# Performance work log

Hardware: AMD Instinct MI355X
Metric: run time of the kernel (lower is better)

Reference implementation:

```python
import jax, jax.numpy as jnp
import numpy as np

N_FEAT = 128
N_HID = 32
N_HEAD = 4
N_CLASS = 40
HIDDEN = N_HID * N_HEAD  # 128
N_NODES = 50000
N_EDGES = 800000


def _gat_layer(x, src, dst, W, a_s, a_d, b, heads, out_ch, concat):
    # PyG GATConv (eval mode, self-loops already appended to src/dst).
    N = x.shape[0]
    h = (x @ W).reshape(N, heads, out_ch)                      # [N,H,C]
    es = jnp.einsum('nhc,hc->nh', h, a_s)                      # alpha_src per node
    ed = jnp.einsum('nhc,hc->nh', h, a_d)                      # alpha_dst per node
    e = jax.nn.leaky_relu(es[src] + ed[dst], 0.2)              # [E,H]
    m = jax.ops.segment_max(e, dst, num_segments=N)            # segment softmax over dst
    p = jnp.exp(e - m[dst])
    s = jax.ops.segment_sum(p, dst, num_segments=N)
    alpha = p / s[dst]                                         # [E,H]
    out = jax.ops.segment_sum(h[src] * alpha[:, :, None], dst, num_segments=N)  # [N,H,C]
    out = out.reshape(N, heads * out_ch) if concat else out.mean(axis=1)
    return out + b


def setup_inputs() -> dict:
    key = jax.random.key(0)
    ks = jax.random.split(key, 16)
    sc = 0.1
    inp = {
        'x': jax.random.normal(ks[0], (N_NODES, N_FEAT), jnp.float32),
        'edge_index': jax.random.randint(ks[1], (2, N_EDGES), 0, N_NODES, jnp.int32),
        'W0': jax.random.normal(ks[2], (N_FEAT, HIDDEN), jnp.float32) * sc,
        'as0': jax.random.normal(ks[3], (N_HEAD, N_HID), jnp.float32) * sc,
        'ad0': jax.random.normal(ks[4], (N_HEAD, N_HID), jnp.float32) * sc,
        'b0': jnp.zeros((HIDDEN,), jnp.float32),
        'W1': jax.random.normal(ks[5], (HIDDEN, HIDDEN), jnp.float32) * sc,
        'as1': jax.random.normal(ks[6], (N_HEAD, N_HID), jnp.float32) * sc,
        'ad1': jax.random.normal(ks[7], (N_HEAD, N_HID), jnp.float32) * sc,
        'b1': jnp.zeros((HIDDEN,), jnp.float32),
        'W2': jax.random.normal(ks[8], (HIDDEN, HIDDEN), jnp.float32) * sc,
        'as2': jax.random.normal(ks[9], (N_HEAD, N_HID), jnp.float32) * sc,
        'ad2': jax.random.normal(ks[10], (N_HEAD, N_HID), jnp.float32) * sc,
        'b2': jnp.zeros((HIDDEN,), jnp.float32),
        'Wo': jax.random.normal(ks[11], (HIDDEN, N_CLASS), jnp.float32) * sc,
        'aso': jax.random.normal(ks[12], (1, N_CLASS), jnp.float32) * sc,
        'ado': jax.random.normal(ks[13], (1, N_CLASS), jnp.float32) * sc,
        'bo': jnp.zeros((N_CLASS,), jnp.float32),
    }
    return inp


def reference(x, edge_index, W0, as0, ad0, b0, W1, as1, ad1, b1, W2, as2, ad2, b2, Wo, aso, ado, bo):
    N = x.shape[0]
    loops = jnp.arange(N, dtype=edge_index.dtype)              # add_self_loops=True
    src = jnp.concatenate([edge_index[0], loops])
    dst = jnp.concatenate([edge_index[1], loops])
    # dropout is a no-op in eval mode
    x = jax.nn.elu(_gat_layer(x, src, dst, W0, as0, ad0, b0, N_HEAD, N_HID, True))
    for (W, a1, a2, b) in ((W1, as1, ad1, b1), (W2, as2, ad2, b2)):
        h = _gat_layer(x, src, dst, W, a1, a2, b, N_HEAD, N_HID, True)
        x = jax.nn.elu(h + x)                                  # 'res' skip connection
    out = _gat_layer(x, src, dst, Wo, aso, ado, bo, 1, N_CLASS, False)
    return out
```

## Files before the change

kernel.cpp:

```cpp
#include <hip/hip_runtime.h>
#include <hip/hip_bf16.h>

#define N_FEAT 128
#define HIDDEN 128
#define NHEAD  4
#define NHID   32
#define NCLASS 40


__global__ __launch_bounds__(256) void k_zero(int* __restrict__ p, int n) {
  int i = blockIdx.x * 256 + threadIdx.x;
  if (i < n) p[i] = 0;
}

__global__ __launch_bounds__(256) void k_hist(const int* __restrict__ dst, int* __restrict__ counts, int E) {
  int e = blockIdx.x * 256 + threadIdx.x;
  if (e < E) atomicAdd(&counts[dst[e]], 1);
}

__device__ __forceinline__ int block_incl_scan_256(int v, int* sm) {
  int t = threadIdx.x;
  sm[t] = v;
  __syncthreads();
  #pragma unroll
  for (int d = 1; d < 256; d <<= 1) {
    int u = (t >= d) ? sm[t - d] : 0;
    __syncthreads();
    sm[t] += u;
    __syncthreads();
  }
  return sm[t];
}

__global__ __launch_bounds__(256) void k_bsum(const int* __restrict__ counts, int* __restrict__ bsum, int N) {
  __shared__ int sm[256];
  int i = blockIdx.x * 256 + threadIdx.x;
  int v = (i < N) ? counts[i] : 0;
  int incl = block_incl_scan_256(v, sm);
  if (threadIdx.x == 255) bsum[blockIdx.x] = incl;
}

__global__ __launch_bounds__(256) void k_scanb(const int* __restrict__ bsum, int* __restrict__ boff,
                                               int* __restrict__ offs, int nblk, int N) {
  __shared__ int sm[256];
  int t = threadIdx.x;
  int v = (t < nblk) ? bsum[t] : 0;
  int incl = block_incl_scan_256(v, sm);
  if (t < nblk) boff[t] = incl - v;
  if (t == 255) offs[N] = incl;
}

__global__ __launch_bounds__(256) void k_scanfin(const int* __restrict__ counts, const int* __restrict__ boff,
                                                 int* __restrict__ offs, int* __restrict__ cursor, int N) {
  __shared__ int sm[256];
  int b = blockIdx.x;
  int i = b * 256 + threadIdx.x;
  int v = (i < N) ? counts[i] : 0;
  int incl = block_incl_scan_256(v, sm);
  int excl = incl - v + boff[b];
  if (i < N) {
    offs[i] = excl;
    cursor[i] = excl;
  }
}

__global__ __launch_bounds__(256) void k_scatter(const int* __restrict__ src, const int* __restrict__ dst,
                                                 int* __restrict__ cursor, int* __restrict__ csr_src, int E) {
  int e = blockIdx.x * 256 + threadIdx.x;
  if (e < E) {
    int d = dst[e];
    int pos = atomicAdd(&cursor[d], 1);
    csr_src[pos] = src[e];
  }
}

__device__ __forceinline__ unsigned short f2bf(float x) {
  unsigned int u = __float_as_uint(x);
  u += 0x7fffu + ((u >> 16) & 1u);
  return (unsigned short)(u >> 16);
}


__global__ __launch_bounds__(256) void k_gemm128(const float* __restrict__ X, const float* __restrict__ W,
                                                 const float* __restrict__ a_s, const float* __restrict__ a_d,
                                                 unsigned short* __restrict__ Hb16, float* __restrict__ es,
                                                 float* __restrict__ ed, int N) {
  __shared__ float xs[32][132];
  int row0 = blockIdx.x * 32;
  int tid = threadIdx.x;
  for (int i = tid; i < 1024; i += 256) {
    int r = i >> 5, c4 = i & 31;
    int row = row0 + r;
    float4 v = make_float4(0.f, 0.f, 0.f, 0.f);
    if (row < N) v = *reinterpret_cast<const float4*>(X + (size_t)row * 128 + c4 * 4);
    *reinterpret_cast<float4*>(&xs[r][c4 * 4]) = v;
  }
  __syncthreads();
  int tc = tid & 31;
  int tr = tid >> 5;
  float acc[4][4] = {};
  const float* Wp = W + tc * 4;
  #pragma unroll 4
  for (int k = 0; k < 128; ++k) {
    float4 w = *reinterpret_cast<const float4*>(Wp + (size_t)k * 128);
    float x0 = xs[tr][k], x1 = xs[tr + 8][k], x2 = xs[tr + 16][k], x3 = xs[tr + 24][k];
    acc[0][0] += x0 * w.x; acc[0][1] += x0 * w.y; acc[0][2] += x0 * w.z; acc[0][3] += x0 * w.w;
    acc[1][0] += x1 * w.x; acc[1][1] += x1 * w.y; acc[1][2] += x1 * w.z; acc[1][3] += x1 * w.w;
    acc[2][0] += x2 * w.x; acc[2][1] += x2 * w.y; acc[2][2] += x2 * w.z; acc[2][3] += x2 * w.w;
    acc[3][0] += x3 * w.x; acc[3][1] += x3 * w.y; acc[3][2] += x3 * w.z; acc[3][3] += x3 * w.w;
  }
  #pragma unroll
  for (int m = 0; m < 4; ++m) {
    int row = row0 + tr + 8 * m;
    if (row < N) {
      ushort4 b = make_ushort4(f2bf(acc[m][0]), f2bf(acc[m][1]), f2bf(acc[m][2]), f2bf(acc[m][3]));
      *reinterpret_cast<ushort4*>(Hb16 + (size_t)row * 128 + tc * 4) = b;
    }
  }
  __syncthreads();
  #pragma unroll
  for (int m = 0; m < 4; ++m)
    *reinterpret_cast<float4*>(&xs[tr + 8 * m][tc * 4]) =
        make_float4(acc[m][0], acc[m][1], acc[m][2], acc[m][3]);
  __syncthreads();
  if (tid < 128) {
    int r = tid >> 2, hd = tid & 3;
    int row = row0 + r;
    if (row < N) {
      const float* asp = a_s + hd * NHID;
      const float* adp = a_d + hd * NHID;
      float s1 = 0.f, s2 = 0.f;
      #pragma unroll
      for (int c = 0; c < NHID; ++c) {
        float v = xs[r][hd * NHID + c];
        s1 += v * asp[c];
        s2 += v * adp[c];
      }
      es[row * NHEAD + hd] = s1;
      ed[row * NHEAD + hd] = s2;
    }
  }
}

__global__ __launch_bounds__(256) void k_gemm40(const float* __restrict__ X, const float* __restrict__ W,
                                                const float* __restrict__ a_s, const float* __restrict__ a_d,
                                                float* __restrict__ H, float* __restrict__ es,
                                                float* __restrict__ ed, int N) {
  __shared__ float xs[32][132];
  __shared__ float ws[128 * 40];
  int row0 = blockIdx.x * 32;
  int tid = threadIdx.x;
  for (int i = tid; i < 1024; i += 256) {
    int r = i >> 5, c4 = i & 31;
    int row = row0 + r;
    float4 v = make_float4(0.f, 0.f, 0.f, 0.f);
    if (row < N) v = *reinterpret_cast<const float4*>(X + (size_t)row * 128 + c4 * 4);
    *reinterpret_cast<float4*>(&xs[r][c4 * 4]) = v;
  }
  for (int i = tid; i < 1280; i += 256)
    *reinterpret_cast<float4*>(&ws[i * 4]) = *reinterpret_cast<const float4*>(W + i * 4);
  __syncthreads();
  int r = tid >> 3;
  int cg = tid & 7;
  float acc[5] = {};
  #pragma unroll 4
  for (int k = 0; k < 128; ++k) {
    float xv = xs[r][k];
    #pragma unroll
    for (int j = 0; j < 5; ++j) acc[j] += xv * ws[k * 40 + cg * 5 + j];
  }
  int row = row0 + r;
  if (row < N) {
    #pragma unroll
    for (int j = 0; j < 5; ++j) H[(size_t)row * 40 + cg * 5 + j] = acc[j];
  }
  __syncthreads();
  #pragma unroll
  for (int j = 0; j < 5; ++j) xs[r][cg * 5 + j] = acc[j];
  __syncthreads();
  if (tid < 32) {
    int rr = tid;
    int rw = row0 + rr;
    if (rw < N) {
      float s1 = 0.f, s2 = 0.f;
      #pragma unroll
      for (int c = 0; c < NCLASS; ++c) {
        float v = xs[rr][c];
        s1 += v * a_s[c];
        s2 += v * a_d[c];
      }
      es[rw] = s1;
      ed[rw] = s2;
    }
  }
}


__device__ __forceinline__ float lrelu02(float x) { return x > 0.f ? x : 0.2f * x; }

template <int CTOT, int HEADS, int MODE, bool BF16>
__global__ __launch_bounds__(256) void k_agg(const void* __restrict__ hv, const float* __restrict__ es,
                                             const float* __restrict__ ed, const int* __restrict__ offs,
                                             const int* __restrict__ csr_src, const float* __restrict__ bias,
                                             const float* __restrict__ x_in, float* __restrict__ out, int N) {
  int wid = (blockIdx.x * 256 + threadIdx.x) >> 6;
  int lane = threadIdx.x & 63;
  if (wid >= N) return;
  constexpr int CH = CTOT / HEADS;
  constexpr int PAIRS = CTOT / 2;
  const float* hf = (const float*)hv;
  const unsigned short* hb = (const unsigned short*)hv;
  int n = wid;
  int c = 2 * lane;
  bool act = lane < PAIRS;
  int hd = act ? (c / CH) : 0;
  float edv = ed[n * HEADS + hd];
  float acc0 = 0.f, acc1 = 0.f, sp = 0.f;
  int beg = offs[n], end = offs[n + 1];
  int i = beg;
  for (; i + 8 <= end; i += 8) {
    int sA[8];
    #pragma unroll
    for (int u = 0; u < 8; ++u) sA[u] = csr_src[i + u];
    float eA[8];
    #pragma unroll
    for (int u = 0; u < 8; ++u) eA[u] = es[sA[u] * HEADS + hd];
    float hx[8], hy[8];
    if (BF16) {
      #pragma unroll
      for (int u = 0; u < 8; ++u) {
        unsigned int v = act ? *reinterpret_cast<const unsigned int*>(hb + (size_t)sA[u] * CTOT + c) : 0u;
        hx[u] = __uint_as_float(v << 16);
        hy[u] = __uint_as_float(v & 0xffff0000u);
      }
    } else {
      #pragma unroll
      for (int u = 0; u < 8; ++u) {
        float2 t = act ? *reinterpret_cast<const float2*>(hf + (size_t)sA[u] * CTOT + c)
                       : make_float2(0.f, 0.f);
        hx[u] = t.x;
        hy[u] = t.y;
      }
    }
    #pragma unroll
    for (int u = 0; u < 8; ++u) {
      float p = __expf(lrelu02(eA[u] + edv));
      sp += p;
      acc0 += p * hx[u];
      acc1 += p * hy[u];
    }
  }
  for (; i <= end; ++i) {
    int s = (i < end) ? csr_src[i] : n;
    float p = __expf(lrelu02(es[s * HEADS + hd] + edv));
    sp += p;
    if (act) {
      float vx, vy;
      if (BF16) {
        unsigned int v = *reinterpret_cast<const unsigned int*>(hb + (size_t)s * CTOT + c);
        vx = __uint_as_float(v << 16);
        vy = __uint_as_float(v & 0xffff0000u);
      } else {
        float2 t = *reinterpret_cast<const float2*>(hf + (size_t)s * CTOT + c);
        vx = t.x;
        vy = t.y;
      }
      acc0 += p * vx;
      acc1 += p * vy;
    }
  }
  if (act) {
    float v0 = acc0 / sp + bias[c];
    float v1 = acc1 / sp + bias[c + 1];
    if (MODE == 1) {
      float2 xv = *reinterpret_cast<const float2*>(x_in + (size_t)n * CTOT + c);
      v0 += xv.x;
      v1 += xv.y;
    }
    if (MODE != 2) {
      v0 = v0 > 0.f ? v0 : __expf(v0) - 1.f;
      v1 = v1 > 0.f ? v1 : __expf(v1) - 1.f;
    }
    *reinterpret_cast<float2*>(out + (size_t)n * CTOT + c) = make_float2(v0, v1);
  }
}


extern "C" void kernel_launch(void* const* d_in, const int* in_sizes, int n_in,
                              void* d_out, int out_size, void* d_ws, size_t ws_size,
                              hipStream_t stream) {
  const float* X   = (const float*)d_in[0];
  const int*   EI  = (const int*)d_in[1];
  const float* W0  = (const float*)d_in[2];
  const float* AS0 = (const float*)d_in[3];
  const float* AD0 = (const float*)d_in[4];
  const float* B0  = (const float*)d_in[5];
  const float* W1  = (const float*)d_in[6];
  const float* AS1 = (const float*)d_in[7];
  const float* AD1 = (const float*)d_in[8];
  const float* B1  = (const float*)d_in[9];
  const float* W2  = (const float*)d_in[10];
  const float* AS2 = (const float*)d_in[11];
  const float* AD2 = (const float*)d_in[12];
  const float* B2  = (const float*)d_in[13];
  const float* WO  = (const float*)d_in[14];
  const float* ASO = (const float*)d_in[15];
  const float* ADO = (const float*)d_in[16];
  const float* BO  = (const float*)d_in[17];

  int N = in_sizes[0] / N_FEAT;
  int E = in_sizes[1] / 2;
  const int* srcv = EI;
  const int* dstv = EI + E;

  char* w = (char*)d_ws;
  auto alloc = [&](size_t bytes) {
    char* p = w;
    w += (bytes + 255) & ~(size_t)255;
    return p;
  };
  int*            offs    = (int*)alloc((size_t)(N + 1) * sizeof(int));
  int*            cursor  = (int*)alloc((size_t)N * sizeof(int));
  int*            csr_src = (int*)alloc((size_t)E * sizeof(int));
  float*          es      = (float*)alloc((size_t)N * NHEAD * sizeof(float));
  float*          ed      = (float*)alloc((size_t)N * NHEAD * sizeof(float));
  float*          xb      = (float*)alloc((size_t)N * HIDDEN * sizeof(float));
  unsigned short* hb16    = (unsigned short*)alloc((size_t)N * HIDDEN * sizeof(unsigned short));
  float*          hb      = (float*)alloc((size_t)N * NCLASS * sizeof(float));
  int*            bsum    = (int*)alloc(256 * sizeof(int));
  int*            boff    = (int*)alloc(256 * sizeof(int));
  (void)ws_size;

  int egrid = (E + 255) / 256;
  int ngrid = (N + 255) / 256;
  int ggrid = (N + 31) / 32;
  int agrid = (N + 3) / 4;
  int sblk  = (N + 255) / 256;

  k_zero<<<ngrid, 256, 0, stream>>>(cursor, N);
  k_hist<<<egrid, 256, 0, stream>>>(dstv, cursor, E);
  k_bsum<<<sblk, 256, 0, stream>>>(cursor, bsum, N);
  k_scanb<<<1, 256, 0, stream>>>(bsum, boff, offs, sblk, N);
  k_scanfin<<<sblk, 256, 0, stream>>>(cursor, boff, offs, cursor, N);
  k_scatter<<<egrid, 256, 0, stream>>>(srcv, dstv, cursor, csr_src, E);

  k_gemm128<<<ggrid, 256, 0, stream>>>(X, W0, AS0, AD0, hb16, es, ed, N);
  k_agg<HIDDEN, NHEAD, 0, true><<<agrid, 256, 0, stream>>>(hb16, es, ed, offs, csr_src, B0, nullptr, xb, N);
  k_gemm128<<<ggrid, 256, 0, stream>>>(xb, W1, AS1, AD1, hb16, es, ed, N);
  k_agg<HIDDEN, NHEAD, 1, true><<<agrid, 256, 0, stream>>>(hb16, es, ed, offs, csr_src, B1, xb, xb, N);
  k_gemm128<<<ggrid, 256, 0, stream>>>(xb, W2, AS2, AD2, hb16, es, ed, N);
  k_agg<HIDDEN, NHEAD, 1, true><<<agrid, 256, 0, stream>>>(hb16, es, ed, offs, csr_src, B2, xb, xb, N);
  k_gemm40<<<ggrid, 256, 0, stream>>>(xb, WO, ASO, ADO, hb, es, ed, N);
  k_agg<NCLASS, 1, 2, false><<<agrid, 256, 0, stream>>>(hb, es, ed, offs, csr_src, BO, nullptr, (float*)d_out, N);
}
```

Measured before the change: 538.8 us.

## Use bf16 MFMA for 128-wide GEMM and bf16 features in output layer

Rewrites the 128x128 projection GEMM to convert X and a transposed W to bf16 in shared memory and compute with 16x16x32 bf16 MFMA instructions over 64-row tiles. The attention scores are now computed from bf16-rounded outputs. The final 40-class layer also stores its projected features in bf16, so its aggregation gathers half the bytes. This removes scalar FP32 FMA work and cuts gather bandwidth, at the cost of extra precision loss on inputs and the attention logits.

```diff
diff --git a/kernel.cpp b/kernel.cpp
--- a/kernel.cpp
+++ b/kernel.cpp
@@ -6,6 +6,9 @@
 #define NHEAD  4
 #define NHID   32
 #define NCLASS 40
+
+typedef __attribute__((ext_vector_type(8))) short short8v;
+typedef __attribute__((ext_vector_type(4))) float float4v;
 
 
 __global__ __launch_bounds__(256) void k_zero(int* __restrict__ p, int n) {
@@ -79,51 +82,68 @@
   u += 0x7fffu + ((u >> 16) & 1u);
   return (unsigned short)(u >> 16);
 }
-
+__device__ __forceinline__ float bf2f(unsigned short b) {
+  return __uint_as_float(((unsigned int)b) << 16);
+}
 
 __global__ __launch_bounds__(256) void k_gemm128(const float* __restrict__ X, const float* __restrict__ W,
                                                  const float* __restrict__ a_s, const float* __restrict__ a_d,
                                                  unsigned short* __restrict__ Hb16, float* __restrict__ es,
                                                  float* __restrict__ ed, int N) {
-  __shared__ float xs[32][132];
-  int row0 = blockIdx.x * 32;
+  __shared__ unsigned short xa[64][136];
+  __shared__ unsigned short wt[128][136];
+  int row0 = blockIdx.x * 64;
   int tid = threadIdx.x;
-  for (int i = tid; i < 1024; i += 256) {
-    int r = i >> 5, c4 = i & 31;
+  #pragma unroll
+  for (int i = 0; i < 8; ++i) {
+    int idx = i * 256 + tid;
+    int r = idx >> 5, c4 = idx & 31;
     int row = row0 + r;
     float4 v = make_float4(0.f, 0.f, 0.f, 0.f);
     if (row < N) v = *reinterpret_cast<const float4*>(X + (size_t)row * 128 + c4 * 4);
-    *reinterpret_cast<float4*>(&xs[r][c4 * 4]) = v;
-  }
-  __syncthreads();
-  int tc = tid & 31;
-  int tr = tid >> 5;
-  float acc[4][4] = {};
-  const float* Wp = W + tc * 4;
-  #pragma unroll 4
-  for (int k = 0; k < 128; ++k) {
-    float4 w = *reinterpret_cast<const float4*>(Wp + (size_t)k * 128);
-    float x0 = xs[tr][k], x1 = xs[tr + 8][k], x2 = xs[tr + 16][k], x3 = xs[tr + 24][k];
-    acc[0][0] += x0 * w.x; acc[0][1] += x0 * w.y; acc[0][2] += x0 * w.z; acc[0][3] += x0 * w.w;
-    acc[1][0] += x1 * w.x; acc[1][1] += x1 * w.y; acc[1][2] += x1 * w.z; acc[1][3] += x1 * w.w;
-    acc[2][0] += x2 * w.x; acc[2][1] += x2 * w.y; acc[2][2] += x2 * w.z; acc[2][3] += x2 * w.w;
-    acc[3][0] += x3 * w.x; acc[3][1] += x3 * w.y; acc[3][2] += x3 * w.z; acc[3][3] += x3 * w.w;
-  }
-  #pragma unroll
-  for (int m = 0; m < 4; ++m) {
-    int row = row0 + tr + 8 * m;
-    if (row < N) {
-      ushort4 b = make_ushort4(f2bf(acc[m][0]), f2bf(acc[m][1]), f2bf(acc[m][2]), f2bf(acc[m][3]));
-      *reinterpret_cast<ushort4*>(Hb16 + (size_t)row * 128 + tc * 4) = b;
-    }
-  }
-  __syncthreads();
-  #pragma unroll
-  for (int m = 0; m < 4; ++m)
-    *reinterpret_cast<float4*>(&xs[tr + 8 * m][tc * 4]) =
-        make_float4(acc[m][0], acc[m][1], acc[m][2], acc[m][3]);
-  __syncthreads();
-  if (tid < 128) {
+    ushort4 b = make_ushort4(f2bf(v.x), f2bf(v.y), f2bf(v.z), f2bf(v.w));
+    *reinterpret_cast<ushort4*>(&xa[r][c4 * 4]) = b;
+  }
+  #pragma unroll
+  for (int i = 0; i < 16; ++i) {
+    int idx = i * 256 + tid;
+    int k = idx & 127, j4 = idx >> 7;
+    float4 v = *reinterpret_cast<const float4*>(W + (size_t)k * 128 + j4 * 4);
+    wt[j4 * 4 + 0][k] = f2bf(v.x);
+    wt[j4 * 4 + 1][k] = f2bf(v.y);
+    wt[j4 * 4 + 2][k] = f2bf(v.z);
+    wt[j4 * 4 + 3][k] = f2bf(v.w);
+  }
+  __syncthreads();
+  int l = tid & 63, wv = tid >> 6;
+  int lrow = l & 15, lk = l >> 4;
+  short8v a[4];
+  #pragma unroll
+  for (int kk = 0; kk < 4; ++kk)
+    a[kk] = *reinterpret_cast<const short8v*>(&xa[wv * 16 + lrow][kk * 32 + lk * 8]);
+  #pragma unroll
+  for (int ct = 0; ct < 8; ++ct) {
+    float4v acc = {0.f, 0.f, 0.f, 0.f};
+    #pragma unroll
+    for (int kk = 0; kk < 4; ++kk) {
+      short8v b = *reinterpret_cast<const short8v*>(&wt[ct * 16 + lrow][kk * 32 + lk * 8]);
+      acc = __builtin_amdgcn_mfma_f32_16x16x32_bf16(a[kk], b, acc, 0, 0, 0);
+    }
+    #pragma unroll
+    for (int r = 0; r < 4; ++r)
+      xa[wv * 16 + lk * 4 + r][ct * 16 + lrow] = f2bf(acc[r]);
+  }
+  __syncthreads();
+  #pragma unroll
+  for (int i = 0; i < 8; ++i) {
+    int idx = i * 256 + tid;
+    int r = idx >> 5, c4 = idx & 31;
+    int row = row0 + r;
+    if (row < N)
+      *reinterpret_cast<ushort4*>(Hb16 + (size_t)row * 128 + c4 * 4) =
+          *reinterpret_cast<const ushort4*>(&xa[r][c4 * 4]);
+  }
+  {
     int r = tid >> 2, hd = tid & 3;
     int row = row0 + r;
     if (row < N) {
@@ -132,7 +152,7 @@
       float s1 = 0.f, s2 = 0.f;
       #pragma unroll
       for (int c = 0; c < NHID; ++c) {
-        float v = xs[r][hd * NHID + c];
+        float v = bf2f(xa[r][hd * NHID + c]);
         s1 += v * asp[c];
         s2 += v * adp[c];
       }
@@ -144,7 +164,7 @@
 
 __global__ __launch_bounds__(256) void k_gemm40(const float* __restrict__ X, const float* __restrict__ W,
                                                 const float* __restrict__ a_s, const float* __restrict__ a_d,
-                                                float* __restrict__ H, float* __restrict__ es,
+                                                unsigned short* __restrict__ Hb16, float* __restrict__ es,
                                                 float* __restrict__ ed, int N) {
   __shared__ float xs[32][132];
   __shared__ float ws[128 * 40];
@@ -172,7 +192,7 @@
   int row = row0 + r;
   if (row < N) {
     #pragma unroll
-    for (int j = 0; j < 5; ++j) H[(size_t)row * 40 + cg * 5 + j] = acc[j];
+    for (int j = 0; j < 5; ++j) Hb16[(size_t)row * 40 + cg * 5 + j] = f2bf(acc[j]);
   }
   __syncthreads();
   #pragma unroll
@@ -326,14 +346,15 @@
   float*          ed      = (float*)alloc((size_t)N * NHEAD * sizeof(float));
   float*          xb      = (float*)alloc((size_t)N * HIDDEN * sizeof(float));
   unsigned short* hb16    = (unsigned short*)alloc((size_t)N * HIDDEN * sizeof(unsigned short));
-  float*          hb      = (float*)alloc((size_t)N * NCLASS * sizeof(float));
+  unsigned short* ho16    = (unsigned short*)alloc((size_t)N * NCLASS * sizeof(unsigned short));
   int*            bsum    = (int*)alloc(256 * sizeof(int));
   int*            boff    = (int*)alloc(256 * sizeof(int));
   (void)ws_size;
 
   int egrid = (E + 255) / 256;
   int ngrid = (N + 255) / 256;
-  int ggrid = (N + 31) / 32;
+  int ggrid = (N + 63) / 64;
+  int g40   = (N + 31) / 32;
   int agrid = (N + 3) / 4;
   int sblk  = (N + 255) / 256;
 
@@ -350,6 +371,6 @@
   k_agg<HIDDEN, NHEAD, 1, true><<<agrid, 256, 0, stream>>>(hb16, es, ed, offs, csr_src, B1, xb, xb, N);
   k_gemm128<<<ggrid, 256, 0, stream>>>(xb, W2, AS2, AD2, hb16, es, ed, N);
   k_agg<HIDDEN, NHEAD, 1, true><<<agrid, 256, 0, stream>>>(hb16, es, ed, offs, csr_src, B2, xb, xb, N);
-  k_gemm40<<<ggrid, 256, 0, stream>>>(xb, WO, ASO, ADO, hb, es, ed, N);
-  k_agg<NCLASS, 1, 2, false><<<agrid, 256, 0, stream>>>(hb, es, ed, offs, csr_src, BO, nullptr, (float*)d_out, N);
-}
+  k_gemm40<<<g40, 256, 0, stream>>>(xb, WO, ASO, ADO, ho16, es, ed, N);
+  k_agg<NCLASS, 1, 2, true><<<agrid, 256, 0, stream>>>(ho16, es, ed, offs, csr_src, BO, nullptr, (float*)d_out, N);
+}
```

Measured after the change: 482.5 us. -10.5%, faster.
